# Kernel optimization log

Measured on AMD Instinct MI355X. Metric: run time of the kernel, lower is better.

## Reference

```python
import jax, jax.numpy as jnp
import numpy as np


def _chamfer(x1, x2):
    """Squared-L2 chamfer distances.
    x1: [B,N,3], x2: [B,M,3]
    returns dist1: [B,N] (min over x2), dist2: [B,M] (min over x1).
    """
    sq1 = jnp.sum(x1 * x1, axis=-1)           # [B,N]
    sq2 = jnp.sum(x2 * x2, axis=-1)           # [B,M]
    cross = jnp.einsum('bnd,bmd->bnm', x1, x2)  # [B,N,M]
    d = sq1[:, :, None] + sq2[:, None, :] - 2.0 * cross
    dist1 = jnp.min(d, axis=2)
    dist2 = jnp.min(d, axis=1)
    return dist1, dist2


def setup_inputs() -> dict:
    key = jax.random.key(0)
    k1, k2, k3 = jax.random.split(key, 3)
    partial = jax.random.normal(k1, (4, 2048, 3), dtype=jnp.float32)
    infer = jax.random.normal(k2, (4, 8192, 3), dtype=jnp.float32)
    complete = jax.random.normal(k3, (4, 8192, 3), dtype=jnp.float32)
    return {"partial": partial, "infer": infer, "complete": complete}


def reference(partial, infer, complete):
    # dist_cp: per-complete-point min sq-dist to partial
    _, dist_cp = _chamfer(partial, complete)
    # dist_ic: per-infer-point min sq-dist to complete; dist_ci: per-complete min to infer
    dist_ic, dist_ci = _chamfer(infer, complete)
    max_dist_cp = jnp.max(dist_cp)
    weighted_dist_ci = dist_cp * dist_ci / max_dist_cp
    return jnp.mean(dist_ic) + jnp.mean(weighted_dist_ci)
```

## Files before the change

kernel.cpp:

```cpp
#include <hip/hip_runtime.h>


#define BATCH 4
#define NP    2048
#define NQ    8192
#define NTOT  (BATCH*NQ)
#define ONEB  0x3F80u

typedef float v16f __attribute__((ext_vector_type(16)));
typedef short v8s  __attribute__((ext_vector_type(8)));
union U4S8 { uint4 u; v8s s; };

__device__ __forceinline__ unsigned int bfr(float f) {
    unsigned int u = __float_as_uint(f);
    u += 0x7FFFu + ((u >> 16) & 1u);
    return (u >> 16);
}
__device__ __forceinline__ float bff(unsigned int h) {
    return __uint_as_float(h << 16);
}

__device__ __forceinline__ v8s buildA32(const float* qp, int half) {
    float qx = qp[0], qy = qp[1], qz = qp[2];
    unsigned xh = bfr(qx), yh = bfr(qy), zh = bfr(qz);
    unsigned xl = bfr(qx - bff(xh)), yl = bfr(qy - bff(yh)), zl = bfr(qz - bff(zh));
    float s = fmaf(qx, qx, fmaf(qy, qy, qz*qz));
    unsigned sh = bfr(s), sl = bfr(s - bff(sh));
    unsigned mxh = bfr(-2.0f*bff(xh)), myh = bfr(-2.0f*bff(yh)), mzh = bfr(-2.0f*bff(zh));
    unsigned mxl = bfr(-2.0f*bff(xl)), myl = bfr(-2.0f*bff(yl)), mzl = bfr(-2.0f*bff(zl));
    uint4 q0 = make_uint4(mxh | (myh<<16), mzh | (mxh<<16), myh | (mzh<<16), mxl | (myl<<16));
    uint4 q1 = make_uint4(mzl | (ONEB<<16), ONEB | (sh<<16), sl, 0u);
    U4S8 r;
    r.u.x = half ? q1.x : q0.x;
    r.u.y = half ? q1.y : q0.y;
    r.u.z = half ? q1.z : q0.z;
    r.u.w = half ? q1.w : q0.w;
    return r.s;
}

#define R16M(M) M(0) M(1) M(2) M(3) M(4) M(5) M(6) M(7) \
                M(8) M(9) M(10) M(11) M(12) M(13) M(14) M(15)
#define WR(r) { int rw = ((r) & 3) + 8*((r) >> 2) + 4*half; \
                red[rw*33 + n] = mnA[r]; red[1056 + rw*33 + n] = mnB[r]; }

__global__ __launch_bounds__(256, 4) void minDistKernel(
    const float* __restrict__ partial,
    const float* __restrict__ infer,
    const float* __restrict__ complete,
    unsigned int* __restrict__ keys)
{
    __shared__ __align__(16) unsigned char lds[33792];

    const int tid = threadIdx.x;
    const int lane = tid & 63, w = tid >> 6;
    const int half = lane >> 5, n = lane & 31;

    const int x = blockIdx.x, z = blockIdx.z;

    if (x == 0 && z == 0 && tid == 0) {
        keys[3*NTOT + 0] = 0u;
        keys[3*NTOT + 1] = 0u;
        keys[3*NTOT + 2] = 0u;
        keys[3*NTOT + 3] = 0u;
    }

    int cid, task;
    if (z < 2)       { task = 0; cid = z; }
    else if (z < 10) { task = 1; cid = z - 2; }
    else             { task = 2; cid = z - 10; }
    const int b = x >> 5;

    const float* qraw; const float* craw; int trow;
    if (task == 0)      { qraw = complete + b*NQ*3; craw = partial  + (b*NP + cid*1024)*3; trow = 0; }
    else if (task == 1) { qraw = infer    + b*NQ*3; craw = complete + (b*NQ + cid*1024)*3; trow = 1; }
    else                { qraw = complete + b*NQ*3; craw = infer    + (b*NQ + cid*1024)*3; trow = 2; }

    {
        const float4* p4 = (const float4*)(craw) + tid*3;
        float4 f0 = p4[0], f1 = p4[1], f2 = p4[2];
        float cs[12] = {f0.x,f0.y,f0.z,f0.w, f1.x,f1.y,f1.z,f1.w, f2.x,f2.y,f2.z,f2.w};
        #pragma unroll
        for (int r = 0; r < 4; ++r) {
            float cx = cs[r*3+0], cy = cs[r*3+1], cz = cs[r*3+2];
            unsigned xh = bfr(cx), yh = bfr(cy), zh = bfr(cz);
            unsigned xl = bfr(cx - bff(xh)), yl = bfr(cy - bff(yh)), zl = bfr(cz - bff(zh));
            float s = fmaf(cx, cx, fmaf(cy, cy, cz*cz));
            unsigned sh = bfr(s), sl = bfr(s - bff(sh));
            int c = tid*4 + r, t = c >> 5, cn = c & 31;
            *(uint4*)(lds + t*1024 + cn*16) =
                make_uint4(xh | (yh<<16), zh | (xl<<16), yl | (zl<<16), xh | (yh<<16));
            *(uint4*)(lds + t*1024 + 512 + cn*16) =
                make_uint4(zh | (sh<<16), sl | (ONEB<<16), ONEB, 0u);
        }
    }

    const int q0 = (x & 31)*256 + w*64;
    v8s a0 = buildA32(qraw + (q0 + n)*3, half);
    v8s a1 = buildA32(qraw + (q0 + 32 + n)*3, half);

    const float INF = __builtin_inff();
    v16f mnA, mnB, Z;
    #pragma unroll
    for (int r = 0; r < 16; ++r) { mnA[r] = INF; mnB[r] = INF; Z[r] = 0.0f; }

    __syncthreads();

    U4S8 c0u, c1u;
    c0u.u = *(const uint4*)(lds + 0*1024 + lane*16);
    c1u.u = *(const uint4*)(lds + 1*1024 + lane*16);
    #pragma unroll 1
    for (int t = 0; t < 32; t += 2) {
        const int tn = (t + 2) & 31;
        U4S8 n0u, n1u;
        n0u.u = *(const uint4*)(lds + tn*1024 + lane*16);
        n1u.u = *(const uint4*)(lds + (tn+1)*1024 + lane*16);

        v8s bf0 = c0u.s, bf1 = c1u.s;
        {
            v16f d0 = __builtin_amdgcn_mfma_f32_32x32x16_bf16(a0, bf0, Z, 0, 0, 0);
            v16f d1 = __builtin_amdgcn_mfma_f32_32x32x16_bf16(a0, bf1, Z, 0, 0, 0);
            #pragma unroll
            for (int r = 0; r < 16; ++r) mnA[r] = fminf(mnA[r], fminf(d0[r], d1[r]));
        }
        {
            v16f d0 = __builtin_amdgcn_mfma_f32_32x32x16_bf16(a1, bf0, Z, 0, 0, 0);
            v16f d1 = __builtin_amdgcn_mfma_f32_32x32x16_bf16(a1, bf1, Z, 0, 0, 0);
            #pragma unroll
            for (int r = 0; r < 16; ++r) mnB[r] = fminf(mnB[r], fminf(d0[r], d1[r]));
        }
        c0u = n0u; c1u = n1u;
    }

    __syncthreads();
    float* red = (float*)lds + w*2112;
    R16M(WR)
    __syncthreads();

    const float* myrow = red + half*1056 + n*33;
    float p0 = myrow[0], p1 = myrow[1], p2 = myrow[2], p3 = myrow[3];
    #pragma unroll
    for (int j = 4; j < 32; j += 4) {
        p0 = fminf(p0, myrow[j+0]); p1 = fminf(p1, myrow[j+1]);
        p2 = fminf(p2, myrow[j+2]); p3 = fminf(p3, myrow[j+3]);
    }
    float m = fminf(fminf(p0, p1), fminf(p2, p3));

    unsigned int* krow = keys + trow*NTOT + b*NQ;
    atomicMin(&krow[q0 + half*32 + n], __float_as_uint(fmaxf(m, 0.0f)));
}

__global__ __launch_bounds__(256) void reduceKernel(
    unsigned int* __restrict__ keys, float* __restrict__ out)
{
    const int tid = threadIdx.x;
    const int i = blockIdx.x * 256 + tid;
    const uint4* kcp = (const uint4*)(keys);
    const uint4* kic = (const uint4*)(keys + NTOT);
    const uint4* kci = (const uint4*)(keys + 2*NTOT);
    unsigned int* scr = keys + 3*NTOT;

    uint4 a = kcp[i]; uint4 bb = kic[i]; uint4 c = kci[i];
    float a0 = __uint_as_float(a.x),  a1 = __uint_as_float(a.y);
    float a2 = __uint_as_float(a.z),  a3 = __uint_as_float(a.w);
    float mx = fmaxf(fmaxf(a0, a1), fmaxf(a2, a3));
    float s1 = (__uint_as_float(bb.x) + __uint_as_float(bb.y))
             + (__uint_as_float(bb.z) + __uint_as_float(bb.w));
    float s2 = fmaf(a0, __uint_as_float(c.x), fmaf(a1, __uint_as_float(c.y),
               fmaf(a2, __uint_as_float(c.z), a3 * __uint_as_float(c.w))));

    #pragma unroll
    for (int off = 32; off > 0; off >>= 1) {
        mx = fmaxf(mx, __shfl_down(mx, off));
        s1 += __shfl_down(s1, off);
        s2 += __shfl_down(s2, off);
    }

    __shared__ float smx[4], ss1[4], ss2[4];
    const int wid = tid >> 6, lane = tid & 63;
    if (lane == 0) { smx[wid] = mx; ss1[wid] = s1; ss2[wid] = s2; }
    __syncthreads();

    if (tid == 0) {
        float M = fmaxf(fmaxf(smx[0], smx[1]), fmaxf(smx[2], smx[3]));
        float S1 = (ss1[0] + ss1[1]) + (ss1[2] + ss1[3]);
        float S2 = (ss2[0] + ss2[1]) + (ss2[2] + ss2[3]);
        atomicMax(&scr[1], __float_as_uint(M));
        atomicAdd((float*)&scr[2], S1);
        atomicAdd((float*)&scr[3], S2);
        __threadfence();
        unsigned old = atomicAdd(&scr[0], 1u);
        if (old == 31u) {
            float Mt  = __uint_as_float(atomicOr(&scr[1], 0u));
            float S1t = atomicAdd((float*)&scr[2], 0.0f);
            float S2t = atomicAdd((float*)&scr[3], 0.0f);
            out[0] = S1t / (float)NTOT + S2t / (Mt * (float)NTOT);
        }
    }
}

extern "C" void kernel_launch(void* const* d_in, const int* in_sizes, int n_in,
                              void* d_out, int out_size, void* d_ws, size_t ws_size,
                              hipStream_t stream) {
    const float* partial  = (const float*)d_in[0];
    const float* infer    = (const float*)d_in[1];
    const float* complete = (const float*)d_in[2];
    unsigned int* keys = (unsigned int*)d_ws;

    minDistKernel<<<dim3(128, 1, 18), 256, 0, stream>>>(partial, infer, complete, keys);
    reduceKernel<<<32, 256, 0, stream>>>(keys, (float*)d_out);
}
```

Before: 82.79 us.

## Fuse infer-complete both-direction minima into one MFMA pass with column atomics

The infer→complete and complete→infer tasks computed the same distance matrix twice. The kernel now computes it once, taking row minima as before and also column minima per 32-wide tile through an in-register min tree and LDS atomicMin, then flushes them to global keys with atomicMin. The grid drops from 18 to 10 z-slices, roughly halving the MFMA work. In exchange the fused blocks do extra VALU min reductions and LDS/global atomics, and the LDS-load prefetch across iterations has been removed.

```diff
diff --git a/kernel.cpp b/kernel.cpp
--- a/kernel.cpp
+++ b/kernel.cpp
@@ -38,6 +38,17 @@
     return r.s;
 }
 
+__device__ __forceinline__ float tree16(const v16f& d) {
+    float t0 = fminf(fminf(d[0],  d[1]),  d[2]);
+    float t1 = fminf(fminf(d[3],  d[4]),  d[5]);
+    float t2 = fminf(fminf(d[6],  d[7]),  d[8]);
+    float t3 = fminf(fminf(d[9],  d[10]), d[11]);
+    float t4 = fminf(fminf(d[12], d[13]), d[14]);
+    float t5 = fminf(fminf(t0, t1), d[15]);
+    float t6 = fminf(fminf(t2, t3), t4);
+    return fminf(t5, t6);
+}
+
 #define R16M(M) M(0) M(1) M(2) M(3) M(4) M(5) M(6) M(7) \
                 M(8) M(9) M(10) M(11) M(12) M(13) M(14) M(15)
 #define WR(r) { int rw = ((r) & 3) + 8*((r) >> 2) + 4*half; \
@@ -50,6 +61,7 @@
     unsigned int* __restrict__ keys)
 {
     __shared__ __align__(16) unsigned char lds[33792];
+    __shared__ unsigned int ccol[1024];
 
     const int tid = threadIdx.x;
     const int lane = tid & 63, w = tid >> 6;
@@ -64,16 +76,13 @@
         keys[3*NTOT + 3] = 0u;
     }
 
-    int cid, task;
-    if (z < 2)       { task = 0; cid = z; }
-    else if (z < 10) { task = 1; cid = z - 2; }
-    else             { task = 2; cid = z - 10; }
+    const int fused = (z >= 2);
+    const int cid = fused ? (z - 2) : z;
     const int b = x >> 5;
 
     const float* qraw; const float* craw; int trow;
-    if (task == 0)      { qraw = complete + b*NQ*3; craw = partial  + (b*NP + cid*1024)*3; trow = 0; }
-    else if (task == 1) { qraw = infer    + b*NQ*3; craw = complete + (b*NQ + cid*1024)*3; trow = 1; }
-    else                { qraw = complete + b*NQ*3; craw = infer    + (b*NQ + cid*1024)*3; trow = 2; }
+    if (!fused) { qraw = complete + b*NQ*3; craw = partial  + (b*NP + cid*1024)*3; trow = 0; }
+    else        { qraw = infer    + b*NQ*3; craw = complete + (b*NQ + cid*1024)*3; trow = 1; }
 
     {
         const float4* p4 = (const float4*)(craw) + tid*3;
@@ -93,6 +102,8 @@
                 make_uint4(zh | (sh<<16), sl | (ONEB<<16), ONEB, 0u);
         }
     }
+    #pragma unroll
+    for (int k = 0; k < 4; ++k) ccol[k*256 + tid] = 0x7F800000u;
 
     const int q0 = (x & 31)*256 + w*64;
     v8s a0 = buildA32(qraw + (q0 + n)*3, half);
@@ -105,35 +116,47 @@
 
     __syncthreads();
 
-    U4S8 c0u, c1u;
-    c0u.u = *(const uint4*)(lds + 0*1024 + lane*16);
-    c1u.u = *(const uint4*)(lds + 1*1024 + lane*16);
     #pragma unroll 1
     for (int t = 0; t < 32; t += 2) {
-        const int tn = (t + 2) & 31;
-        U4S8 n0u, n1u;
-        n0u.u = *(const uint4*)(lds + tn*1024 + lane*16);
-        n1u.u = *(const uint4*)(lds + (tn+1)*1024 + lane*16);
-
-        v8s bf0 = c0u.s, bf1 = c1u.s;
+        U4S8 b0u, b1u;
+        b0u.u = *(const uint4*)(lds + t*1024 + lane*16);
+        b1u.u = *(const uint4*)(lds + (t+1)*1024 + lane*16);
+        v8s bf0 = b0u.s, bf1 = b1u.s;
+
+        float cm0, cm1;
         {
             v16f d0 = __builtin_amdgcn_mfma_f32_32x32x16_bf16(a0, bf0, Z, 0, 0, 0);
             v16f d1 = __builtin_amdgcn_mfma_f32_32x32x16_bf16(a0, bf1, Z, 0, 0, 0);
             #pragma unroll
             for (int r = 0; r < 16; ++r) mnA[r] = fminf(mnA[r], fminf(d0[r], d1[r]));
+            if (fused) { cm0 = tree16(d0); cm1 = tree16(d1); }
         }
         {
-            v16f d0 = __builtin_amdgcn_mfma_f32_32x32x16_bf16(a1, bf0, Z, 0, 0, 0);
-            v16f d1 = __builtin_amdgcn_mfma_f32_32x32x16_bf16(a1, bf1, Z, 0, 0, 0);
+            v16f e0 = __builtin_amdgcn_mfma_f32_32x32x16_bf16(a1, bf0, Z, 0, 0, 0);
+            v16f e1 = __builtin_amdgcn_mfma_f32_32x32x16_bf16(a1, bf1, Z, 0, 0, 0);
             #pragma unroll
-            for (int r = 0; r < 16; ++r) mnB[r] = fminf(mnB[r], fminf(d0[r], d1[r]));
-        }
-        c0u = n0u; c1u = n1u;
+            for (int r = 0; r < 16; ++r) mnB[r] = fminf(mnB[r], fminf(e0[r], e1[r]));
+            if (fused) {
+                cm0 = fminf(cm0, tree16(e0));
+                cm1 = fminf(cm1, tree16(e1));
+                atomicMin(&ccol[t*32 + n],     __float_as_uint(fmaxf(cm0, 0.0f)));
+                atomicMin(&ccol[(t+1)*32 + n], __float_as_uint(fmaxf(cm1, 0.0f)));
+            }
+        }
     }
 
     __syncthreads();
     float* red = (float*)lds + w*2112;
     R16M(WR)
+
+    if (fused) {
+        unsigned int* crow2 = keys + 2*NTOT + b*NQ + cid*1024;
+        #pragma unroll
+        for (int k = 0; k < 4; ++k) {
+            int c = k*256 + tid;
+            atomicMin(&crow2[c], ccol[c]);
+        }
+    }
     __syncthreads();
 
     const float* myrow = red + half*1056 + n*33;
@@ -206,6 +229,6 @@
     const float* complete = (const float*)d_in[2];
     unsigned int* keys = (unsigned int*)d_ws;
 
-    minDistKernel<<<dim3(128, 1, 18), 256, 0, stream>>>(partial, infer, complete, keys);
+    minDistKernel<<<dim3(128, 1, 10), 256, 0, stream>>>(partial, infer, complete, keys);
     reduceKernel<<<32, 256, 0, stream>>>(keys, (float*)d_out);
 }
```

New measurement: 80.26 us. 3.1% less time.
